# Kernel tuning notes

Measured on AMD Instinct MI355X. Metric: run time of the kernel, lower is better.

Reference implementation:

```python
import jax, jax.numpy as jnp
import numpy as np

P = 2  # sampling ratio: keep top ceil(M/p) measurements


def setup_inputs() -> dict:
    key = jax.random.key(0)
    k1, k2, k3 = jax.random.split(key, 3)
    B, H, W, C = 8, 1024, 1024, 3
    Y = jax.random.normal(k1, (B, H, W, C), dtype=jnp.float32)
    # build()-time Z0 components: abs ~ N(0.5, 0.1), angle ~ N(0, 0.5*sqrt(pi))
    Z0_abs = 0.5 + 0.1 * jax.random.normal(k2, (1, 1, H, W), dtype=jnp.float32)
    Z0_angle = (0.5 * np.pi ** 0.5) * jax.random.normal(k3, (1, 1, H, W), dtype=jnp.float32)
    return {"Y": Y, "Z0_abs": Z0_abs, "Z0_angle": Z0_angle}


def _make_Z0(Z0_abs, Z0_angle):
    # Z0 = |Z0| * exp(i*angle), Frobenius-normalized over spatial axes (2,3)
    Z0 = Z0_abs.astype(jnp.complex64) * jnp.exp(1j * Z0_angle.astype(jnp.complex64))
    fro = jnp.sqrt(jnp.sum(jnp.abs(Z0) ** 2, axis=(2, 3), keepdims=True)).astype(jnp.complex64)
    return Z0 / fro


def reference(Y, Z0_abs, Z0_angle):
    B, H, W, C = Y.shape
    M = H * W * C
    R = int(np.ceil(M / P))
    # transpose NHWC -> NCHW, scale by original S[2] (= W)
    Y_S = jnp.transpose(Y.astype(jnp.float32), (0, 3, 1, 2)) / jnp.float32(W)
    y_s = Y_S.reshape(B, M)
    # threshold = R-th largest value per batch (== descending-sorted index R-1)
    thr = jax.lax.top_k(y_s, R)[0][:, -1]  # [B]
    Ytr = (Y_S >= thr[:, None, None, None]).astype(jnp.float32)  # [B,C,H,W]
    Z0 = _make_Z0(Z0_abs, Z0_angle)
    return Ytr, Z0
```

## Files before the change

kernel.cpp:

```cpp
#include <hip/hip_runtime.h>
#include <math.h>

#define BATCH 8
#define HH 1024
#define WW 1024
#define CC 3
#define MTOT (HH*WW*CC)
#define RSEL 1572864u
#define CAP  65536u

#define U_HI 0xBC800000u
#define U_LO 0x437FFFFFu

#define WS_CNT_OFF    0u
#define WS_CHI_OFF    64u
#define WS_THR_OFF    128u
#define WS_NORM_OFF   192u
#define WS_ZERO_BYTES 256u
#define WS_BUF_OFF    1024u

__device__ __forceinline__ unsigned int fmap(float x) {
    unsigned int b = __float_as_uint(x);
    return (b & 0x80000000u) ? ~b : (b | 0x80000000u);
}

__global__ void pass1_kernel(const float* __restrict__ Y,
                             unsigned int* __restrict__ buf,
                             unsigned int* __restrict__ cnt,
                             unsigned int* __restrict__ chigh) {
    __shared__ unsigned int lbuf[2048];
    __shared__ unsigned int lcnt;
    __shared__ unsigned int gbase;
    __shared__ unsigned int red[4];
    const int b = blockIdx.y;
    const int tid = threadIdx.x;
    if (tid == 0) lcnt = 0u;
    __syncthreads();

    const float4* Y4 = (const float4*)(Y + (size_t)b * MTOT);
    unsigned int* bbuf = buf + (size_t)b * CAP;
    const int n4 = MTOT / 4;
    const int stride = gridDim.x * blockDim.x;
    const int iters = (n4 + stride - 1) / stride;
    unsigned int hcnt = 0u;

    for (int it = 0; it < iters; it++) {
        int i = it * stride + blockIdx.x * blockDim.x + tid;
        if (i < n4) {
            float4 v = Y4[i];
            unsigned int u;
#define PROC(comp) u = fmap(comp); \
            if (u >= U_HI) hcnt++; \
            else if (u >= U_LO) { unsigned int p = atomicAdd(&lcnt, 1u); if (p < 2048u) lbuf[p] = u; }
            PROC(v.x) PROC(v.y) PROC(v.z) PROC(v.w)
#undef PROC
        }
        __syncthreads();
        if (lcnt >= 1024u) {
            unsigned int n = lcnt;
            if (tid == 0) gbase = atomicAdd(&cnt[b], n);
            __syncthreads();
            for (unsigned int j = tid; j < n; j += blockDim.x) {
                unsigned int p = gbase + j;
                if (p < CAP) bbuf[p] = lbuf[j];
            }
            __syncthreads();
            if (tid == 0) lcnt = 0u;
        }
        __syncthreads();
    }
    unsigned int n = lcnt;
    if (n > 2048u) n = 2048u;
    if (tid == 0 && n > 0u) gbase = atomicAdd(&cnt[b], n);
    __syncthreads();
    for (unsigned int j = tid; j < n; j += blockDim.x) {
        unsigned int p = gbase + j;
        if (p < CAP) bbuf[p] = lbuf[j];
    }
    for (int d = 32; d > 0; d >>= 1) hcnt += __shfl_down(hcnt, d);
    if ((tid & 63) == 0) red[tid >> 6] = hcnt;
    __syncthreads();
    if (tid == 0) atomicAdd(&chigh[b], red[0] + red[1] + red[2] + red[3]);
}

__global__ void __launch_bounds__(1024) refine_kernel(
        const float* __restrict__ Y,
        const unsigned int* __restrict__ buf,
        const unsigned int* __restrict__ cnt,
        const unsigned int* __restrict__ chigh,
        unsigned int* __restrict__ thr) {
    __shared__ unsigned int hist[4096];
    __shared__ unsigned int waveSums[16];
    __shared__ unsigned int selBin, selBase;
    __shared__ unsigned int mode_s, n_s, target_s;
    const int b = blockIdx.x;
    const int tid = threadIdx.x;
    const int lane = tid & 63, wid = tid >> 6;

    if (tid == 0) {
        unsigned int Nw = cnt[b], Ch = chigh[b];
        int fb = (Ch >= RSEL) || (Nw > CAP) || (Ch + Nw < RSEL);
        mode_s = (unsigned int)fb;
        n_s = fb ? (unsigned int)MTOT : Nw;
        target_s = fb ? RSEL : (RSEL - Ch);
    }
    __syncthreads();
    const int fb = (int)mode_s;
    const unsigned int n = n_s;
    unsigned int target = target_s;
    const unsigned int* src = buf + (size_t)b * CAP;
    const float* Yb = Y + (size_t)b * MTOT;

    unsigned int d1 = 0, d2 = 0;

    for (int level = 0; level < 3; level++) {
        const int nb  = (level < 2) ? 4096 : 256;
        const int bpt = (level < 2) ? 4 : 1;
        for (int i = tid; i < nb; i += 1024) hist[i] = 0u;
        __syncthreads();
        for (unsigned int i = tid; i < n; i += 1024u) {
            unsigned int u = fb ? fmap(Yb[i]) : src[i];
            if (level == 0) {
                atomicAdd(&hist[u >> 20], 1u);
            } else if (level == 1) {
                if ((u >> 20) == d1) atomicAdd(&hist[(u >> 8) & 0xFFFu], 1u);
            } else {
                if ((u >> 8) == ((d1 << 12) | d2)) atomicAdd(&hist[u & 0xFFu], 1u);
            }
        }
        __syncthreads();
        unsigned int c[4] = {0u, 0u, 0u, 0u};
        unsigned int s = 0u;
        const int nthr = nb / bpt;
        if (tid < nthr) {
            for (int k = 0; k < bpt; k++) { c[k] = hist[nb - 1 - (tid * bpt + k)]; s += c[k]; }
        }
        unsigned int incl = s;
        for (int d = 1; d < 64; d <<= 1) {
            unsigned int v = __shfl_up(incl, d);
            if (lane >= d) incl += v;
        }
        if (lane == 63) waveSums[wid] = incl;
        __syncthreads();
        if (tid < 16) {
            unsigned int w = waveSums[tid];
            for (int d = 1; d < 16; d <<= 1) {
                unsigned int v = __shfl_up(w, d);
                if (tid >= d) w += v;
            }
            waveSums[tid] = w;
        }
        __syncthreads();
        incl += (wid > 0) ? waveSums[wid - 1] : 0u;
        unsigned int excl = incl - s;
        if (s > 0u && excl < target && incl >= target) {
            unsigned int run = excl;
            for (int k = 0; k < bpt; k++) {
                if (run + c[k] >= target) {
                    selBin = (unsigned int)(nb - 1 - (tid * bpt + k));
                    selBase = run;
                    break;
                }
                run += c[k];
            }
        }
        __syncthreads();
        if (level == 0) d1 = selBin;
        else if (level == 1) d2 = selBin;
        target -= selBase;
        __syncthreads();
    }
    if (tid == 0) thr[b] = (d1 << 20) | (d2 << 8) | selBin;
}

__global__ void thresh_kernel(const float* __restrict__ Y,
                              const unsigned int* __restrict__ thr,
                              float* __restrict__ out) {
    int p = blockIdx.x * blockDim.x + threadIdx.x;
    int w4 = p & 255;
    int h  = (p >> 8) & 1023;
    int b  = p >> 18;
    unsigned int tu = thr[b];
    const float4* src = (const float4*)(Y + ((size_t)((b * HH + h) * WW) + (size_t)w4 * 4) * CC);
    float4 a0 = src[0], a1 = src[1], a2 = src[2];
    float4 r0, r1, r2;
    r0.x = (fmap(a0.x) >= tu) ? 1.f : 0.f;
    r0.y = (fmap(a0.w) >= tu) ? 1.f : 0.f;
    r0.z = (fmap(a1.z) >= tu) ? 1.f : 0.f;
    r0.w = (fmap(a2.y) >= tu) ? 1.f : 0.f;
    r1.x = (fmap(a0.y) >= tu) ? 1.f : 0.f;
    r1.y = (fmap(a1.x) >= tu) ? 1.f : 0.f;
    r1.z = (fmap(a1.w) >= tu) ? 1.f : 0.f;
    r1.w = (fmap(a2.z) >= tu) ? 1.f : 0.f;
    r2.x = (fmap(a0.z) >= tu) ? 1.f : 0.f;
    r2.y = (fmap(a1.y) >= tu) ? 1.f : 0.f;
    r2.z = (fmap(a2.x) >= tu) ? 1.f : 0.f;
    r2.w = (fmap(a2.w) >= tu) ? 1.f : 0.f;
    size_t base = ((size_t)(b * CC) * HH + h) * WW;
    ((float4*)(out + base))[w4]                        = r0;
    ((float4*)(out + base + (size_t)HH * WW))[w4]      = r1;
    ((float4*)(out + base + (size_t)2 * HH * WW))[w4]  = r2;
}

__global__ void znorm_reduce(const float* __restrict__ zabs, float* __restrict__ acc) {
    float s = 0.f;
    const int n4 = HH * WW / 4;
    for (int i = blockIdx.x * blockDim.x + threadIdx.x; i < n4; i += gridDim.x * blockDim.x) {
        float4 v = ((const float4*)zabs)[i];
        s += v.x * v.x + v.y * v.y + v.z * v.z + v.w * v.w;
    }
    for (int off = 32; off > 0; off >>= 1) s += __shfl_down(s, off);
    __shared__ float ls[4];
    if ((threadIdx.x & 63) == 0) ls[threadIdx.x >> 6] = s;
    __syncthreads();
    if (threadIdx.x == 0) atomicAdd(acc, ls[0] + ls[1] + ls[2] + ls[3]);
}

__global__ void zwrite_kernel(const float* __restrict__ zabs,
                              const float* __restrict__ zang,
                              const float* __restrict__ acc,
                              float* __restrict__ outz, int interleaved) {
    int i = blockIdx.x * blockDim.x + threadIdx.x;
    if (i >= HH * WW / 2) return;
    float inv = 1.0f / sqrtf(*acc);
    float2 a = ((const float2*)zabs)[i];
    float2 g = ((const float2*)zang)[i];
    float s0, c0, s1, c1;
    __sincosf(g.x, &s0, &c0);
    __sincosf(g.y, &s1, &c1);
    if (interleaved) {
        float4 o;
        o.x = a.x * c0 * inv; o.y = a.x * s0 * inv;
        o.z = a.y * c1 * inv; o.w = a.y * s1 * inv;
        ((float4*)outz)[i] = o;
    } else {
        float2 o;
        o.x = a.x * c0 * inv; o.y = a.y * c1 * inv;
        ((float2*)outz)[i] = o;
    }
}

extern "C" void kernel_launch(void* const* d_in, const int* in_sizes, int n_in,
                              void* d_out, int out_size, void* d_ws, size_t ws_size,
                              hipStream_t stream) {
    const float* Y    = (const float*)d_in[0];
    const float* zabs = (const float*)d_in[1];
    const float* zang = (const float*)d_in[2];
    float* out = (float*)d_out;

    unsigned char* ws = (unsigned char*)d_ws;
    unsigned int* cnt   = (unsigned int*)(ws + WS_CNT_OFF);
    unsigned int* chigh = (unsigned int*)(ws + WS_CHI_OFF);
    unsigned int* thr   = (unsigned int*)(ws + WS_THR_OFF);
    float*        norm  = (float*)(ws + WS_NORM_OFF);
    unsigned int* buf   = (unsigned int*)(ws + WS_BUF_OFF);

    hipMemsetAsync(d_ws, 0, WS_ZERO_BYTES, stream);

    dim3 fullgrid(96, BATCH);
    pass1_kernel<<<fullgrid, 256, 0, stream>>>(Y, buf, cnt, chigh);
    refine_kernel<<<BATCH, 1024, 0, stream>>>(Y, buf, cnt, chigh, thr);

    thresh_kernel<<<(BATCH * HH * (WW / 4)) / 256, 256, 0, stream>>>(Y, thr, out);

    znorm_reduce<<<256, 256, 0, stream>>>(zabs, norm);
    size_t zoff = (size_t)BATCH * CC * HH * WW;
    int zfloats = out_size - (int)zoff;
    int interleaved = (zfloats >= 2 * HH * WW) ? 1 : 0;
    zwrite_kernel<<<(HH * WW / 2 + 255) / 256, 256, 0, stream>>>(
        zabs, zang, norm, out + zoff, interleaved);
}
```

Measured before the change: 254.3 us.

## Fuse Z0 norm/write into selection kernels and drop memset via per-segment buffers

Replaces the global atomic candidate counters with fixed per-block segment buffers and per-block counts, which removes the memset and the global atomics. The Z0 norm reduction is folded into pass1 as an extra grid row and finished by an extra block in refine. The threshold write and the Z write are merged into one launch. This cuts the launch count from six to three, at the cost of a binary search over segment offsets for every candidate read in refine and a smaller per-segment capacity that can force the full-data fallback.

New measurement: 297.5 us. 1.17x slower.

```diff
diff --git a/kernel.cpp b/kernel.cpp
--- a/kernel.cpp
+++ b/kernel.cpp
@@ -7,17 +7,18 @@
 #define CC 3
 #define MTOT (HH*WW*CC)
 #define RSEL 1572864u
-#define CAP  65536u
+#define NSEG 96
+#define SEGCAP 3072u
 
 #define U_HI 0xBC800000u
 #define U_LO 0x437FFFFFu
 
-#define WS_CNT_OFF    0u
-#define WS_CHI_OFF    64u
-#define WS_THR_OFF    128u
-#define WS_NORM_OFF   192u
-#define WS_ZERO_BYTES 256u
-#define WS_BUF_OFF    1024u
+#define WS_SCNT_OFF   0u
+#define WS_CHI_OFF    4096u
+#define WS_NPART_OFF  8192u
+#define WS_THR_OFF    12288u
+#define WS_NORM_OFF   12352u
+#define WS_BUF_OFF    16384u
 
 __device__ __forceinline__ unsigned int fmap(float x) {
     unsigned int b = __float_as_uint(x);
@@ -25,45 +26,61 @@
 }
 
 __global__ void pass1_kernel(const float* __restrict__ Y,
+                             const float* __restrict__ zabs,
                              unsigned int* __restrict__ buf,
-                             unsigned int* __restrict__ cnt,
-                             unsigned int* __restrict__ chigh) {
+                             unsigned int* __restrict__ scnt,
+                             unsigned int* __restrict__ chi,
+                             float* __restrict__ npart) {
+    const int tid = threadIdx.x;
+    const int bx = blockIdx.x;
+
+    if (blockIdx.y == 8) {
+        float s = 0.f;
+        const int n4z = HH * WW / 4;
+        for (int i = bx * blockDim.x + tid; i < n4z; i += NSEG * blockDim.x) {
+            float4 v = ((const float4*)zabs)[i];
+            s += v.x * v.x + v.y * v.y + v.z * v.z + v.w * v.w;
+        }
+        for (int d = 32; d > 0; d >>= 1) s += __shfl_down(s, d);
+        __shared__ float ls[4];
+        if ((tid & 63) == 0) ls[tid >> 6] = s;
+        __syncthreads();
+        if (tid == 0) npart[bx] = ls[0] + ls[1] + ls[2] + ls[3];
+        return;
+    }
+
     __shared__ unsigned int lbuf[2048];
     __shared__ unsigned int lcnt;
-    __shared__ unsigned int gbase;
     __shared__ unsigned int red[4];
     const int b = blockIdx.y;
-    const int tid = threadIdx.x;
     if (tid == 0) lcnt = 0u;
     __syncthreads();
 
     const float4* Y4 = (const float4*)(Y + (size_t)b * MTOT);
-    unsigned int* bbuf = buf + (size_t)b * CAP;
+    unsigned int* seg = buf + (size_t)(b * NSEG + bx) * SEGCAP;
     const int n4 = MTOT / 4;
-    const int stride = gridDim.x * blockDim.x;
-    const int iters = (n4 + stride - 1) / stride;
+    const int stride = NSEG * blockDim.x;
+    const int iters = n4 / stride;
     unsigned int hcnt = 0u;
+    unsigned int base = 0u;
 
     for (int it = 0; it < iters; it++) {
-        int i = it * stride + blockIdx.x * blockDim.x + tid;
-        if (i < n4) {
-            float4 v = Y4[i];
-            unsigned int u;
+        int i = it * stride + bx * blockDim.x + tid;
+        float4 v = Y4[i];
+        unsigned int u;
 #define PROC(comp) u = fmap(comp); \
-            if (u >= U_HI) hcnt++; \
-            else if (u >= U_LO) { unsigned int p = atomicAdd(&lcnt, 1u); if (p < 2048u) lbuf[p] = u; }
-            PROC(v.x) PROC(v.y) PROC(v.z) PROC(v.w)
+        if (u >= U_HI) hcnt++; \
+        else if (u >= U_LO) { unsigned int p = atomicAdd(&lcnt, 1u); if (p < 2048u) lbuf[p] = u; }
+        PROC(v.x) PROC(v.y) PROC(v.z) PROC(v.w)
 #undef PROC
-        }
-        __syncthreads();
-        if (lcnt >= 1024u) {
-            unsigned int n = lcnt;
-            if (tid == 0) gbase = atomicAdd(&cnt[b], n);
-            __syncthreads();
+        __syncthreads();
+        unsigned int n = lcnt;
+        if (n >= 1024u) {
             for (unsigned int j = tid; j < n; j += blockDim.x) {
-                unsigned int p = gbase + j;
-                if (p < CAP) bbuf[p] = lbuf[j];
-            }
+                unsigned int p = base + j;
+                if (p < SEGCAP) seg[p] = lbuf[j];
+            }
+            base += n;
             __syncthreads();
             if (tid == 0) lcnt = 0u;
         }
@@ -71,44 +88,66 @@
     }
     unsigned int n = lcnt;
     if (n > 2048u) n = 2048u;
-    if (tid == 0 && n > 0u) gbase = atomicAdd(&cnt[b], n);
-    __syncthreads();
     for (unsigned int j = tid; j < n; j += blockDim.x) {
-        unsigned int p = gbase + j;
-        if (p < CAP) bbuf[p] = lbuf[j];
-    }
+        unsigned int p = base + j;
+        if (p < SEGCAP) seg[p] = lbuf[j];
+    }
+    base += lcnt;
+    if (tid == 0) scnt[b * NSEG + bx] = base;
+
     for (int d = 32; d > 0; d >>= 1) hcnt += __shfl_down(hcnt, d);
     if ((tid & 63) == 0) red[tid >> 6] = hcnt;
     __syncthreads();
-    if (tid == 0) atomicAdd(&chigh[b], red[0] + red[1] + red[2] + red[3]);
+    if (tid == 0) chi[b * NSEG + bx] = red[0] + red[1] + red[2] + red[3];
 }
 
 __global__ void __launch_bounds__(1024) refine_kernel(
         const float* __restrict__ Y,
         const unsigned int* __restrict__ buf,
-        const unsigned int* __restrict__ cnt,
-        const unsigned int* __restrict__ chigh,
-        unsigned int* __restrict__ thr) {
+        const unsigned int* __restrict__ scnt,
+        const unsigned int* __restrict__ chi,
+        const float* __restrict__ npart,
+        unsigned int* __restrict__ thr,
+        float* __restrict__ normsum) {
+    const int tid = threadIdx.x;
+
+    if (blockIdx.x == 8) {
+        if (tid == 0) {
+            float s = 0.f;
+            for (int i = 0; i < NSEG; i++) s += npart[i];
+            *normsum = s;
+        }
+        return;
+    }
+
     __shared__ unsigned int hist[4096];
+    __shared__ unsigned int segoff[NSEG + 1];
     __shared__ unsigned int waveSums[16];
     __shared__ unsigned int selBin, selBase;
     __shared__ unsigned int mode_s, n_s, target_s;
     const int b = blockIdx.x;
-    const int tid = threadIdx.x;
     const int lane = tid & 63, wid = tid >> 6;
 
     if (tid == 0) {
-        unsigned int Nw = cnt[b], Ch = chigh[b];
-        int fb = (Ch >= RSEL) || (Nw > CAP) || (Ch + Nw < RSEL);
+        unsigned int run = 0u, Ch = 0u, mx = 0u;
+        for (int j = 0; j < NSEG; j++) {
+            segoff[j] = run;
+            unsigned int c = scnt[b * NSEG + j];
+            if (c > mx) mx = c;
+            run += c;
+            Ch += chi[b * NSEG + j];
+        }
+        segoff[NSEG] = run;
+        int fb = (mx > SEGCAP) || (Ch >= RSEL) || (Ch + run < RSEL);
         mode_s = (unsigned int)fb;
-        n_s = fb ? (unsigned int)MTOT : Nw;
+        n_s = fb ? (unsigned int)MTOT : run;
         target_s = fb ? RSEL : (RSEL - Ch);
     }
     __syncthreads();
     const int fb = (int)mode_s;
     const unsigned int n = n_s;
     unsigned int target = target_s;
-    const unsigned int* src = buf + (size_t)b * CAP;
+    const unsigned int* bseg = buf + (size_t)b * NSEG * SEGCAP;
     const float* Yb = Y + (size_t)b * MTOT;
 
     unsigned int d1 = 0, d2 = 0;
@@ -117,9 +156,17 @@
         const int nb  = (level < 2) ? 4096 : 256;
         const int bpt = (level < 2) ? 4 : 1;
         for (int i = tid; i < nb; i += 1024) hist[i] = 0u;
+        if (tid == 0) { selBin = 0u; selBase = 0u; }
         __syncthreads();
         for (unsigned int i = tid; i < n; i += 1024u) {
-            unsigned int u = fb ? fmap(Yb[i]) : src[i];
+            unsigned int u;
+            if (fb) {
+                u = fmap(Yb[i]);
+            } else {
+                int lo = 0, hi = NSEG - 1;
+                while (lo < hi) { int mid = (lo + hi + 1) >> 1; if (segoff[mid] <= i) lo = mid; else hi = mid - 1; }
+                u = bseg[(size_t)lo * SEGCAP + (i - segoff[lo])];
+            }
             if (level == 0) {
                 atomicAdd(&hist[u >> 20], 1u);
             } else if (level == 1) {
@@ -132,9 +179,8 @@
         unsigned int c[4] = {0u, 0u, 0u, 0u};
         unsigned int s = 0u;
         const int nthr = nb / bpt;
-        if (tid < nthr) {
+        if (tid < nthr)
             for (int k = 0; k < bpt; k++) { c[k] = hist[nb - 1 - (tid * bpt + k)]; s += c[k]; }
-        }
         unsigned int incl = s;
         for (int d = 1; d < 64; d <<= 1) {
             unsigned int v = __shfl_up(incl, d);
@@ -173,70 +219,56 @@
     if (tid == 0) thr[b] = (d1 << 20) | (d2 << 8) | selBin;
 }
 
-__global__ void thresh_kernel(const float* __restrict__ Y,
-                              const unsigned int* __restrict__ thr,
-                              float* __restrict__ out) {
-    int p = blockIdx.x * blockDim.x + threadIdx.x;
-    int w4 = p & 255;
-    int h  = (p >> 8) & 1023;
-    int b  = p >> 18;
-    unsigned int tu = thr[b];
-    const float4* src = (const float4*)(Y + ((size_t)((b * HH + h) * WW) + (size_t)w4 * 4) * CC);
-    float4 a0 = src[0], a1 = src[1], a2 = src[2];
-    float4 r0, r1, r2;
-    r0.x = (fmap(a0.x) >= tu) ? 1.f : 0.f;
-    r0.y = (fmap(a0.w) >= tu) ? 1.f : 0.f;
-    r0.z = (fmap(a1.z) >= tu) ? 1.f : 0.f;
-    r0.w = (fmap(a2.y) >= tu) ? 1.f : 0.f;
-    r1.x = (fmap(a0.y) >= tu) ? 1.f : 0.f;
-    r1.y = (fmap(a1.x) >= tu) ? 1.f : 0.f;
-    r1.z = (fmap(a1.w) >= tu) ? 1.f : 0.f;
-    r1.w = (fmap(a2.z) >= tu) ? 1.f : 0.f;
-    r2.x = (fmap(a0.z) >= tu) ? 1.f : 0.f;
-    r2.y = (fmap(a1.y) >= tu) ? 1.f : 0.f;
-    r2.z = (fmap(a2.x) >= tu) ? 1.f : 0.f;
-    r2.w = (fmap(a2.w) >= tu) ? 1.f : 0.f;
-    size_t base = ((size_t)(b * CC) * HH + h) * WW;
-    ((float4*)(out + base))[w4]                        = r0;
-    ((float4*)(out + base + (size_t)HH * WW))[w4]      = r1;
-    ((float4*)(out + base + (size_t)2 * HH * WW))[w4]  = r2;
-}
-
-__global__ void znorm_reduce(const float* __restrict__ zabs, float* __restrict__ acc) {
-    float s = 0.f;
-    const int n4 = HH * WW / 4;
-    for (int i = blockIdx.x * blockDim.x + threadIdx.x; i < n4; i += gridDim.x * blockDim.x) {
-        float4 v = ((const float4*)zabs)[i];
-        s += v.x * v.x + v.y * v.y + v.z * v.z + v.w * v.w;
-    }
-    for (int off = 32; off > 0; off >>= 1) s += __shfl_down(s, off);
-    __shared__ float ls[4];
-    if ((threadIdx.x & 63) == 0) ls[threadIdx.x >> 6] = s;
-    __syncthreads();
-    if (threadIdx.x == 0) atomicAdd(acc, ls[0] + ls[1] + ls[2] + ls[3]);
-}
-
-__global__ void zwrite_kernel(const float* __restrict__ zabs,
-                              const float* __restrict__ zang,
-                              const float* __restrict__ acc,
-                              float* __restrict__ outz, int interleaved) {
-    int i = blockIdx.x * blockDim.x + threadIdx.x;
-    if (i >= HH * WW / 2) return;
-    float inv = 1.0f / sqrtf(*acc);
-    float2 a = ((const float2*)zabs)[i];
-    float2 g = ((const float2*)zang)[i];
-    float s0, c0, s1, c1;
-    __sincosf(g.x, &s0, &c0);
-    __sincosf(g.y, &s1, &c1);
-    if (interleaved) {
-        float4 o;
-        o.x = a.x * c0 * inv; o.y = a.x * s0 * inv;
-        o.z = a.y * c1 * inv; o.w = a.y * s1 * inv;
-        ((float4*)outz)[i] = o;
+__global__ void thresh_z_kernel(const float* __restrict__ Y,
+                                const unsigned int* __restrict__ thr,
+                                const float* __restrict__ zabs,
+                                const float* __restrict__ zang,
+                                const float* __restrict__ normsum,
+                                float* __restrict__ out,
+                                float* __restrict__ outz, int interleaved) {
+    if (blockIdx.x < 8192) {
+        int p = blockIdx.x * blockDim.x + threadIdx.x;
+        int w4 = p & 255;
+        int h  = (p >> 8) & 1023;
+        int b  = p >> 18;
+        unsigned int tu = thr[b];
+        const float4* src = (const float4*)(Y + ((size_t)((b * HH + h) * WW) + (size_t)w4 * 4) * CC);
+        float4 a0 = src[0], a1 = src[1], a2 = src[2];
+        float4 r0, r1, r2;
+        r0.x = (fmap(a0.x) >= tu) ? 1.f : 0.f;
+        r0.y = (fmap(a0.w) >= tu) ? 1.f : 0.f;
+        r0.z = (fmap(a1.z) >= tu) ? 1.f : 0.f;
+        r0.w = (fmap(a2.y) >= tu) ? 1.f : 0.f;
+        r1.x = (fmap(a0.y) >= tu) ? 1.f : 0.f;
+        r1.y = (fmap(a1.x) >= tu) ? 1.f : 0.f;
+        r1.z = (fmap(a1.w) >= tu) ? 1.f : 0.f;
+        r1.w = (fmap(a2.z) >= tu) ? 1.f : 0.f;
+        r2.x = (fmap(a0.z) >= tu) ? 1.f : 0.f;
+        r2.y = (fmap(a1.y) >= tu) ? 1.f : 0.f;
+        r2.z = (fmap(a2.x) >= tu) ? 1.f : 0.f;
+        r2.w = (fmap(a2.w) >= tu) ? 1.f : 0.f;
+        size_t base = ((size_t)(b * CC) * HH + h) * WW;
+        ((float4*)(out + base))[w4]                        = r0;
+        ((float4*)(out + base + (size_t)HH * WW))[w4]      = r1;
+        ((float4*)(out + base + (size_t)2 * HH * WW))[w4]  = r2;
     } else {
-        float2 o;
-        o.x = a.x * c0 * inv; o.y = a.y * c1 * inv;
-        ((float2*)outz)[i] = o;
+        int i = (blockIdx.x - 8192) * blockDim.x + threadIdx.x;
+        float inv = 1.0f / sqrtf(*normsum);
+        float2 a = ((const float2*)zabs)[i];
+        float2 g = ((const float2*)zang)[i];
+        float s0, c0, s1, c1;
+        __sincosf(g.x, &s0, &c0);
+        __sincosf(g.y, &s1, &c1);
+        if (interleaved) {
+            float4 o;
+            o.x = a.x * c0 * inv; o.y = a.x * s0 * inv;
+            o.z = a.y * c1 * inv; o.w = a.y * s1 * inv;
+            ((float4*)outz)[i] = o;
+        } else {
+            float2 o;
+            o.x = a.x * c0 * inv; o.y = a.y * c1 * inv;
+            ((float2*)outz)[i] = o;
+        }
     }
 }
 
@@ -249,24 +281,20 @@
     float* out = (float*)d_out;
 
     unsigned char* ws = (unsigned char*)d_ws;
-    unsigned int* cnt   = (unsigned int*)(ws + WS_CNT_OFF);
-    unsigned int* chigh = (unsigned int*)(ws + WS_CHI_OFF);
+    unsigned int* scnt  = (unsigned int*)(ws + WS_SCNT_OFF);
+    unsigned int* chi   = (unsigned int*)(ws + WS_CHI_OFF);
+    float*        npart = (float*)(ws + WS_NPART_OFF);
     unsigned int* thr   = (unsigned int*)(ws + WS_THR_OFF);
     float*        norm  = (float*)(ws + WS_NORM_OFF);
     unsigned int* buf   = (unsigned int*)(ws + WS_BUF_OFF);
 
-    hipMemsetAsync(d_ws, 0, WS_ZERO_BYTES, stream);
-
-    dim3 fullgrid(96, BATCH);
-    pass1_kernel<<<fullgrid, 256, 0, stream>>>(Y, buf, cnt, chigh);
-    refine_kernel<<<BATCH, 1024, 0, stream>>>(Y, buf, cnt, chigh, thr);
-
-    thresh_kernel<<<(BATCH * HH * (WW / 4)) / 256, 256, 0, stream>>>(Y, thr, out);
-
-    znorm_reduce<<<256, 256, 0, stream>>>(zabs, norm);
+    dim3 g1(NSEG, 9);
+    pass1_kernel<<<g1, 256, 0, stream>>>(Y, zabs, buf, scnt, chi, npart);
+    refine_kernel<<<9, 1024, 0, stream>>>(Y, buf, scnt, chi, npart, thr, norm);
+
     size_t zoff = (size_t)BATCH * CC * HH * WW;
     int zfloats = out_size - (int)zoff;
     int interleaved = (zfloats >= 2 * HH * WW) ? 1 : 0;
-    zwrite_kernel<<<(HH * WW / 2 + 255) / 256, 256, 0, stream>>>(
-        zabs, zang, norm, out + zoff, interleaved);
-}
+    thresh_z_kernel<<<8192 + 2048, 256, 0, stream>>>(
+        Y, thr, zabs, zang, norm, out, out + zoff, interleaved);
+}
```
